# Kernel optimization log

Hardware: AMD Instinct MI355X
Metric: run time of the kernel (lower is better)

## Reference

```python
import jax, jax.numpy as jnp
import numpy as np

N = 16384          # input points
F = 128            # feature dim (x is (N, 3+F))
POOL = 4           # pooling_factor
M = N // POOL      # number of FPS query points
K = 16             # num_neighbors


def setup_inputs() -> dict:
    key = jax.random.key(0)
    x = jax.random.normal(key, (N, 3 + F), dtype=jnp.float32)
    return {"x": x}


def _fps(coords, m):
    """Furthest point sampling: coords (N,3) -> m indices. Deterministic start at 0."""
    n = coords.shape[0]

    def step(carry, _):
        min_d2, last = carry
        d2 = jnp.sum((coords - coords[last]) ** 2, axis=-1)  # (N,)
        min_d2 = jnp.minimum(min_d2, d2)
        nxt = jnp.argmax(min_d2).astype(jnp.int32)
        return (min_d2, nxt), nxt

    init = (jnp.full((n,), jnp.inf, dtype=coords.dtype), jnp.int32(0))
    _, idxs = jax.lax.scan(step, init, None, length=m - 1)
    return jnp.concatenate([jnp.zeros((1,), dtype=jnp.int32), idxs])


def reference(x):
    coords = x[:, :3]                          # (N,3)
    fps_idx = _fps(coords, M)                  # (M,)
    q_points = coords[fps_idx]                 # (M,3)

    # knn neighbor query: squared distances (M,N), take K nearest
    d2 = jnp.sum((q_points[:, None, :] - coords[None, :, :]) ** 2, axis=-1)
    _, nbr_idx = jax.lax.top_k(-d2, K)         # (M,K)

    s_feats = x[nbr_idx, 3:]                   # (M,K,F) gather
    pooled = jnp.max(s_feats, axis=1)          # feat_mapping='max' -> (M,F)
    return jnp.concatenate([q_points, pooled], axis=-1)  # (M, 3+F)
```

## Files before the change

### kernel.cpp

```cpp
#include <hip/hip_runtime.h>

#define N_PTS 16384
#define ROWF  131
#define M_OUT 4096
#define KNN   16
#define FPS_T 1024
#define SORT_T 1024

typedef unsigned long long u64;

__device__ __constant__ unsigned short c_spread4[16] =
  {0,1,8,9,64,65,72,73,512,513,520,521,576,577,584,585};

__device__ __forceinline__ int cell_of(float x, float y, float z) {
  int ix = (int)floorf((x + 4.0f) * 2.0f); ix = ix < 0 ? 0 : (ix > 15 ? 15 : ix);
  int iy = (int)floorf((y + 4.0f) * 2.0f); iy = iy < 0 ? 0 : (iy > 15 ? 15 : iy);
  int iz = (int)floorf((z + 4.0f) * 2.0f); iz = iz < 0 ? 0 : (iz > 15 ? 15 : iz);
  return (int)c_spread4[ix] | ((int)c_spread4[iy] << 1) | ((int)c_spread4[iz] << 2);
}

__global__ void prep_kernel(const float* __restrict__ x,
                            float4* __restrict__ coords4) {
  const int p = blockIdx.x * blockDim.x + threadIdx.x;
  if (p < N_PTS) {
    coords4[p] = make_float4(x[p * ROWF + 0], x[p * ROWF + 1],
                             x[p * ROWF + 2], 0.0f);
  }
}

__global__ __launch_bounds__(1024, 1)
void sort_kernel(const float4* __restrict__ coords4, float4* __restrict__ gP4) {
  __shared__ unsigned int sh[4096];
  __shared__ unsigned int sws[16];
  const int tid = threadIdx.x, lane = tid & 63, wid = tid >> 6;

#pragma unroll
  for (int i = 0; i < 4; ++i) sh[tid * 4 + i] = 0;
  __syncthreads();

  int cel[16];
#pragma unroll
  for (int j = 0; j < 16; ++j) {
    const float4 v = coords4[tid + SORT_T * j];
    const int c = cell_of(v.x, v.y, v.z);
    cel[j] = c;
    atomicAdd(&sh[c], 1u);
  }
  __syncthreads();

  const unsigned h0 = sh[tid * 4 + 0], h1 = sh[tid * 4 + 1];
  const unsigned h2 = sh[tid * 4 + 2], h3 = sh[tid * 4 + 3];
  const unsigned tsum = h0 + h1 + h2 + h3;
  unsigned inc = tsum;
#pragma unroll
  for (int off = 1; off < 64; off <<= 1) {
    const unsigned v = __shfl_up(inc, off);
    if (lane >= off) inc += v;
  }
  if (lane == 63) sws[wid] = inc;
  __syncthreads();
  if (tid == 0) {
    unsigned run = 0;
#pragma unroll
    for (int w = 0; w < 16; ++w) { const unsigned t = sws[w]; sws[w] = run; run += t; }
  }
  __syncthreads();
  const unsigned base = sws[wid] + inc - tsum;
  sh[tid * 4 + 0] = base;
  sh[tid * 4 + 1] = base + h0;
  sh[tid * 4 + 2] = base + h0 + h1;
  sh[tid * 4 + 3] = base + h0 + h1 + h2;
  __syncthreads();

#pragma unroll
  for (int j = 0; j < 16; ++j) {
    const int p = tid + SORT_T * j;
    const float4 v = coords4[p];
    const unsigned rk = atomicAdd(&sh[cel[j]], 1u);
    const int slot = (int)(((rk & 15u) << 10) | (rk >> 4));
    gP4[slot] = make_float4(v.x, v.y, v.z, __int_as_float(p));
  }
}

#define REP16(F) F(0) F(1) F(2) F(3) F(4) F(5) F(6) F(7) \
                 F(8) F(9) F(10) F(11) F(12) F(13) F(14) F(15)

__global__
__attribute__((amdgpu_flat_work_group_size(FPS_T, FPS_T)))
__attribute__((amdgpu_waves_per_eu(4, 4)))
void fps_kernel(const float4* __restrict__ coords4,
                const float4* __restrict__ gP4, float* __restrict__ out) {
  __shared__ u64 s_wkey[2][16];
  const int tid = threadIdx.x, lane = tid & 63, wid = tid >> 6;

#define FPS_DECL(j) float px##j, py##j, pz##j, md##j; unsigned ni##j;
  REP16(FPS_DECL)
#undef FPS_DECL

#define FPS_INIT(j) { const float4 v = gP4[(j << 10) + tid];               \
    px##j = v.x; py##j = v.y; pz##j = v.z;                                 \
    ni##j = (unsigned)(N_PTS - 1 - __float_as_int(v.w));                   \
    md##j = __int_as_float(0x7f800000); }
  REP16(FPS_INIT)
#undef FPS_INIT

  float sx = 0.f, sy = 0.f, sz = 0.f;
#define FPS_ACC(j) sx += px##j; sy += py##j; sz += pz##j;
  REP16(FPS_ACC)
#undef FPS_ACC
  const float mx = sx * (1.0f / 16.0f), my = sy * (1.0f / 16.0f),
              mz = sz * (1.0f / 16.0f);
  float r2 = 0.f;
#define FPS_RAD(j) { const float dx = px##j - mx, dy = py##j - my,         \
                     dz = pz##j - mz;                                      \
    r2 = fmaxf(r2, dx * dx + dy * dy + dz * dz); }
  REP16(FPS_RAD)
#undef FPS_RAD
  const float r = sqrtf(r2) * 1.000001f + 1e-6f;

  float u2 = __int_as_float(0x7f800000);
  u64 ckey = 0;

  const float4 q0 = coords4[0];
  float qx = q0.x, qy = q0.y, qz = q0.z;
  if (tid == 0) { out[0] = qx; out[1] = qy; out[2] = qz; }

  for (int s = 1; s < M_OUT; ++s) {
    const float ddx = mx - qx, ddy = my - qy, ddz = mz - qz;
    const float dd = ddx * ddx + ddy * ddy + ddz * ddz;
    const bool skip = (dd * 0.999999f > u2);

    if (!skip) {
      u64 nk = 0;
#define FPS_UPD(j) {                                                       \
      const float dx = px##j - qx, dy = py##j - qy, dz = pz##j - qz;       \
      const float d2 = __fadd_rn(__fadd_rn(__fmul_rn(dx, dx),              \
                                           __fmul_rn(dy, dy)),             \
                                 __fmul_rn(dz, dz));                       \
      const float nm = fminf(md##j, d2);                                   \
      md##j = nm;                                                          \
      const u64 kj = ((u64)__float_as_uint(nm) << 32) | ni##j;             \
      nk = (kj > nk) ? kj : nk; }
      REP16(FPS_UPD)
#undef FPS_UPD
      ckey = nk;
      const float cmax = __uint_as_float((unsigned)(nk >> 32));
      const float u = (sqrtf(cmax * 1.0001f + 1e-12f) + r) * 1.000003f;
      u2 = u * u * 1.000001f;
    }

    u64 k = ckey;
#pragma unroll
    for (int off = 32; off; off >>= 1) {
      const u64 o = __shfl_xor(k, off);
      if (o > k) k = o;
    }
    const int par = s & 1;
    if (lane == 0) s_wkey[par][wid] = k;
    __syncthreads();
    u64 kk = s_wkey[par][lane & 15];
#pragma unroll
    for (int off = 8; off; off >>= 1) {
      const u64 o = __shfl_xor(kk, off);
      if (o > kk) kk = o;
    }
    const int oidx = (N_PTS - 1) - (int)(unsigned)kk;
    const float4 w = coords4[oidx];
    qx = w.x; qy = w.y; qz = w.z;
    if (tid == 0) {
      float* orow = out + (size_t)s * ROWF;
      orow[0] = qx; orow[1] = qy; orow[2] = qz;
    }
  }
}

__global__ __launch_bounds__(256)
void knn_pool_kernel(const float* __restrict__ x,
                     const float4* __restrict__ coords4,
                     float* __restrict__ out) {
  const int lane = threadIdx.x & 63;
  const int q = blockIdx.x * 4 + (threadIdx.x >> 6);

  const float qx = out[(size_t)q * ROWF + 0];
  const float qy = out[(size_t)q * ROWF + 1];
  const float qz = out[(size_t)q * ROWF + 2];

  u64 h[KNN];
#pragma unroll
  for (int k = 0; k < KNN; ++k) h[k] = ~0ULL;

  for (int c = lane; c < N_PTS; c += 64) {
    const float4 v = coords4[c];
    const float dx = v.x - qx, dy = v.y - qy, dz = v.z - qz;
    const float d2 = __fadd_rn(__fadd_rn(__fmul_rn(dx, dx), __fmul_rn(dy, dy)),
                               __fmul_rn(dz, dz));
    const u64 e = ((u64)__float_as_uint(d2) << 32) | (unsigned)c;
    if (e < h[KNN - 1]) {
#pragma unroll
      for (int k = KNN - 1; k >= 1; --k) {
        const u64 prev = h[k - 1];
        h[k] = (e < prev) ? prev : ((e < h[k]) ? e : h[k]);
      }
      h[0] = (e < h[0]) ? e : h[0];
    }
  }

  int nbr[KNN];
#pragma unroll
  for (int rr = 0; rr < KNN; ++rr) {
    u64 best = h[0];
#pragma unroll
    for (int off = 32; off; off >>= 1) {
      const u64 o = __shfl_xor(best, off);
      best = (o < best) ? o : best;
    }
    nbr[rr] = (int)(unsigned)(best & 0xffffffffULL);
    if (h[0] == best) {
#pragma unroll
      for (int k = 0; k < KNN - 1; ++k) h[k] = h[k + 1];
      h[KNN - 1] = ~0ULL;
    }
  }

  float a0 = __int_as_float(0xff800000), a1 = a0;
#pragma unroll
  for (int rr = 0; rr < KNN; ++rr) {
    const float* row = x + (size_t)nbr[rr] * ROWF + 3;
    a0 = fmaxf(a0, row[lane]);
    a1 = fmaxf(a1, row[lane + 64]);
  }
  float* orow = out + (size_t)q * ROWF + 3;
  orow[lane] = a0;
  orow[lane + 64] = a1;
}

extern "C" void kernel_launch(void* const* d_in, const int* in_sizes, int n_in,
                              void* d_out, int out_size, void* d_ws, size_t ws_size,
                              hipStream_t stream) {
  const float* x = (const float*)d_in[0];
  float* out = (float*)d_out;

  float4* coords4 = (float4*)d_ws;
  float4* gP4     = coords4 + N_PTS;

  hipLaunchKernelGGL(prep_kernel, dim3(64), dim3(256), 0, stream, x, coords4);
  hipLaunchKernelGGL(sort_kernel, dim3(1), dim3(1024), 0, stream, coords4, gP4);
  hipLaunchKernelGGL(fps_kernel, dim3(1), dim3(FPS_T), 0, stream,
                     coords4, gP4, out);
  hipLaunchKernelGGL(knn_pool_kernel, dim3(M_OUT / 4), dim3(256), 0, stream,
                     x, coords4, out);
}
```

Before: 7.300 ms.

## Make FPS skip test wave-uniform using per-wave bounding sphere and cached wave max

Measured after the change: 8.089 ms. 10.8% more time.

```diff
diff --git a/kernel.cpp b/kernel.cpp
--- a/kernel.cpp
+++ b/kernel.cpp
@@ -108,29 +108,38 @@
 #define FPS_ACC(j) sx += px##j; sy += py##j; sz += pz##j;
   REP16(FPS_ACC)
 #undef FPS_ACC
-  const float mx = sx * (1.0f / 16.0f), my = sy * (1.0f / 16.0f),
-              mz = sz * (1.0f / 16.0f);
-  float r2 = 0.f;
-#define FPS_RAD(j) { const float dx = px##j - mx, dy = py##j - my,         \
-                     dz = pz##j - mz;                                      \
-    r2 = fmaxf(r2, dx * dx + dy * dy + dz * dz); }
+#pragma unroll
+  for (int off = 32; off; off >>= 1) {
+    sx += __shfl_xor(sx, off);
+    sy += __shfl_xor(sy, off);
+    sz += __shfl_xor(sz, off);
+  }
+  const float wx = sx * (1.0f / 1024.0f), wy = sy * (1.0f / 1024.0f),
+              wz = sz * (1.0f / 1024.0f);
+  float wr2 = 0.f;
+#define FPS_RAD(j) { const float dx = px##j - wx, dy = py##j - wy,         \
+                     dz = pz##j - wz;                                      \
+    wr2 = fmaxf(wr2, dx * dx + dy * dy + dz * dz); }
   REP16(FPS_RAD)
 #undef FPS_RAD
-  const float r = sqrtf(r2) * 1.000001f + 1e-6f;
-
-  float u2 = __int_as_float(0x7f800000);
-  u64 ckey = 0;
+#pragma unroll
+  for (int off = 32; off; off >>= 1)
+    wr2 = fmaxf(wr2, __shfl_xor(wr2, off));
+  const float wr = sqrtf(wr2) * 1.000001f + 1e-6f;
+
+  float wu2 = __int_as_float(0x7f800000);
+  u64 wk = 0;
 
   const float4 q0 = coords4[0];
   float qx = q0.x, qy = q0.y, qz = q0.z;
   if (tid == 0) { out[0] = qx; out[1] = qy; out[2] = qz; }
 
   for (int s = 1; s < M_OUT; ++s) {
-    const float ddx = mx - qx, ddy = my - qy, ddz = mz - qz;
+    const float ddx = wx - qx, ddy = wy - qy, ddz = wz - qz;
     const float dd = ddx * ddx + ddy * ddy + ddz * ddz;
-    const bool skip = (dd * 0.999999f > u2);
-
-    if (!skip) {
+    const int dirty = (dd * 0.999999f <= wu2) ? 1 : 0;
+
+    if (__builtin_amdgcn_readfirstlane(dirty)) {
       u64 nk = 0;
 #define FPS_UPD(j) {                                                       \
       const float dx = px##j - qx, dy = py##j - qy, dz = pz##j - qz;       \
@@ -143,20 +152,19 @@
       nk = (kj > nk) ? kj : nk; }
       REP16(FPS_UPD)
 #undef FPS_UPD
-      ckey = nk;
-      const float cmax = __uint_as_float((unsigned)(nk >> 32));
-      const float u = (sqrtf(cmax * 1.0001f + 1e-12f) + r) * 1.000003f;
-      u2 = u * u * 1.000001f;
-    }
-
-    u64 k = ckey;
-#pragma unroll
-    for (int off = 32; off; off >>= 1) {
-      const u64 o = __shfl_xor(k, off);
-      if (o > k) k = o;
-    }
+#pragma unroll
+      for (int off = 32; off; off >>= 1) {
+        const u64 o = __shfl_xor(nk, off);
+        if (o > nk) nk = o;
+      }
+      wk = nk;
+      const float cmax = __uint_as_float((unsigned)(wk >> 32));
+      const float u = (sqrtf(cmax * 1.0001f + 1e-12f) + wr) * 1.000003f;
+      wu2 = u * u * 1.000001f;
+    }
+
     const int par = s & 1;
-    if (lane == 0) s_wkey[par][wid] = k;
+    if (lane == 0) s_wkey[par][wid] = wk;
     __syncthreads();
     u64 kk = s_wkey[par][lane & 15];
 #pragma unroll
```
